# Kernel tuning notes

Hardware: AMD Instinct MI355X
Metric: run time of the kernel (lower is better)

The kernel has to match this reference:

```python
import jax, jax.numpy as jnp
import numpy as np

B, T, N, H, E, K, HOR, OD = 64, 12, 1024, 64, 16, 3, 12, 1
DIN = 1  # input_dim
EPS = 1e-12


def setup_inputs() -> dict:
    key = jax.random.key(0)
    ks = jax.random.split(key, 8)
    s = 0.02
    return {
        "source": jax.random.normal(ks[0], (B, T, N, DIN), jnp.float32),
        "node_emb": jax.random.normal(ks[1], (N, E), jnp.float32),
        "time_emb": jax.random.normal(ks[2], (T, E), jnp.float32),
        "gate_wp": jax.random.normal(ks[3], (E, K, DIN + H, 2 * H), jnp.float32) * s,
        "gate_bp": jax.random.normal(ks[4], (E, 2 * H), jnp.float32) * s,
        "gate_lng": jnp.ones((E,), jnp.float32),
        "gate_lnb": jnp.zeros((E,), jnp.float32),
        "upd_wp": jax.random.normal(ks[5], (E, K, DIN + H, H), jnp.float32) * s,
        "upd_bp": jax.random.normal(ks[6], (E, H), jnp.float32) * s,
        "upd_lng": jnp.ones((E,), jnp.float32),
        "upd_lnb": jnp.zeros((E,), jnp.float32),
        "out_lng": jnp.ones((H,), jnp.float32),
        "out_lnb": jnp.zeros((H,), jnp.float32),
        "conv_w": jax.random.normal(ks[7], (HOR * OD, H), jnp.float32) * s,
        "conv_b": jnp.zeros((HOR * OD,), jnp.float32),
    }


def _ln(x, g, b):
    m = x.mean(-1, keepdims=True)
    v = x.var(-1, keepdims=True)
    return (x - m) / jnp.sqrt(v + EPS) * g + b


def _dagcn(x, node_emb, t_emb, wp, bp, lng, lnb):
    # x: [B, N, C]; node_emb: [N, E]; t_emb: [E] (one timestep)
    e = _ln(node_emb + t_emb[None, :], lng, lnb)          # [N, E] (dropout off in eval)
    sup = jax.nn.softmax(e @ e.T, axis=1)                  # [N, N]
    sl = [jnp.eye(N, dtype=x.dtype), sup]
    for _ in range(2, K):
        sl.append(2.0 * sup @ sl[-1] - sl[-2])             # Chebyshev recursion
    S = jnp.stack(sl, axis=0)                              # [K, N, N]
    w = jnp.einsum('nd,dkio->nkio', e, wp)                 # per-node weights
    bias = e @ bp                                          # [N, O]
    xg = jnp.einsum('knm,bmc->bnkc', S, x)                 # graph conv
    return jnp.einsum('bnki,nkio->bno', xg, w) + bias


def reference(source, node_emb, time_emb, gate_wp, gate_bp, gate_lng, gate_lnb,
              upd_wp, upd_bp, upd_lng, upd_lnb, out_lng, out_lnb, conv_w, conv_b):
    def step(state, xs):
        x_t, te = xs                                        # [B,N,DIN], [E]
        zr = jax.nn.sigmoid(_dagcn(jnp.concatenate([x_t, state], -1),
                                   node_emb, te, gate_wp, gate_bp, gate_lng, gate_lnb))
        z, r = zr[..., :H], zr[..., H:]
        hc = jnp.tanh(_dagcn(jnp.concatenate([x_t, z * state], -1),
                             node_emb, te, upd_wp, upd_bp, upd_lng, upd_lnb))
        h = r * state + (1.0 - r) * hc
        return h, None

    xs = jnp.swapaxes(source, 0, 1)                        # [T,B,N,DIN]
    h0 = jnp.zeros((B, N, H), source.dtype)
    h, _ = jax.lax.scan(step, h0, (xs, time_emb))          # last hidden state [B,N,H]
    y = _ln(h, out_lng, out_lnb)                           # out_dropout off in eval
    out = jnp.einsum('bnh,oh->bon', y, conv_w) + conv_b[None, :, None]  # end_conv
    return out.reshape(B, HOR, OD, N).transpose(0, 1, 3, 2)  # [B,horizon,N,output_dim]
```

## Files before the change

kernel.cpp:

```cpp
#include <hip/hip_runtime.h>
#include <math.h>

namespace {
constexpr int B_ = 64, T_ = 12, N_ = 1024, H_ = 64, E_ = 16;
constexpr int C_  = 65;
constexpr int BC_ = B_ * C_;
constexpr int OG_ = 128;
constexpr int OU_ = 64;
constexpr float EPS_ = 1e-12f;
constexpr int KP_ = 224;
constexpr int COLG_ = OG_ * KP_;
constexpr int COLU_ = OU_ * KP_;
constexpr int NE_ = N_ * E_;
}

typedef unsigned short u16;
typedef unsigned int u32;
using f16x8 = __attribute__((ext_vector_type(8))) _Float16;
using f16x4 = __attribute__((ext_vector_type(4))) _Float16;
using f32x4 = __attribute__((ext_vector_type(4))) float;

__device__ __forceinline__ u32 div65(u32 x) { return (x * 16135u) >> 20; }

__device__ __forceinline__ void gl_lds16(const void* g, void* l, int lane) {
#if __has_builtin(__builtin_amdgcn_global_load_lds)
  __builtin_amdgcn_global_load_lds((const __attribute__((address_space(1))) u32*)g,
                                   (__attribute__((address_space(3))) u32*)l, 16, 0, 0);
#else
  *(uint4*)((char*)l + lane * 16) = *(const uint4*)g;
#endif
}

__device__ __forceinline__ void wprep_body(const float* __restrict__ wp, int NO,
                                           _Float16* __restrict__ wpC, int k, int tid) {
  if (tid >= NO) return;
  f16x8 lo = {}, hi = {};
  if (k < 195) {
    const u32 seg = div65((u32)k);
    const u32 ii = k - seg * 65;
#pragma unroll
    for (int d = 0; d < 8; d++)
      lo[d] = (_Float16)wp[(((size_t)d * 3 + seg) * 65 + ii) * NO + tid];
#pragma unroll
    for (int d = 0; d < 8; d++)
      hi[d] = (_Float16)wp[(((size_t)(d + 8) * 3 + seg) * 65 + ii) * NO + tid];
  }
  _Float16* dst = &wpC[((size_t)tid * KP_ + k) * 16];
  *(f16x8*)dst = lo;
  *(f16x8*)(dst + 8) = hi;
}

__device__ __forceinline__ void sup_body(const float* __restrict__ eT,
                                         _Float16* __restrict__ s16,
                                         int n, int tid, float* red) {
  float en[E_];
#pragma unroll
  for (int d = 0; d < E_; d++) en[d] = eT[d * N_ + n];
  float lg[4];
  float mx = -3.4e38f;
#pragma unroll
  for (int j = 0; j < 4; j++) {
    int m = tid + 256 * j;
    float s = 0.f;
#pragma unroll
    for (int d = 0; d < E_; d++) s = fmaf(en[d], eT[d * N_ + m], s);
    lg[j] = s;
    mx = fmaxf(mx, s);
  }
  red[tid] = mx; __syncthreads();
  for (int off = 128; off > 0; off >>= 1) {
    if (tid < off) red[tid] = fmaxf(red[tid], red[tid + off]);
    __syncthreads();
  }
  mx = red[0]; __syncthreads();
  float sum = 0.f;
#pragma unroll
  for (int j = 0; j < 4; j++) { lg[j] = __expf(lg[j] - mx); sum += lg[j]; }
  red[tid] = sum; __syncthreads();
  for (int off = 128; off > 0; off >>= 1) {
    if (tid < off) red[tid] += red[tid + off];
    __syncthreads();
  }
  float inv = 1.0f / red[0];
#pragma unroll
  for (int j = 0; j < 4; j++)
    s16[(size_t)n * N_ + tid + 256 * j] = (_Float16)(lg[j] * inv);
}

__device__ __forceinline__ void wgen_body(const float* __restrict__ e,
                                          const _Float16* __restrict__ wpC, int COLS,
                                          _Float16* __restrict__ Wt,
                                          int xb, int yb, int tid, float (*es)[16]) {
  const int col0 = xb * 1024 + tid * 4;
  const int n0 = yb * 64;
#pragma unroll
  for (int q = 0; q < 4; q++) {
    int idx = tid + q * 256;
    es[idx >> 4][idx & 15] = e[(size_t)n0 * 16 + idx];
  }
  __syncthreads();
  float wc[4][16];
#pragma unroll
  for (int cc = 0; cc < 4; cc++) {
    f16x8 a = *(const f16x8*)&wpC[(size_t)(col0 + cc) * 16];
    f16x8 b = *(const f16x8*)&wpC[(size_t)(col0 + cc) * 16 + 8];
#pragma unroll
    for (int d = 0; d < 8; d++) { wc[cc][d] = (float)a[d]; wc[cc][8 + d] = (float)b[d]; }
  }
  for (int nn = 0; nn < 64; nn++) {
    float acc[4] = {};
#pragma unroll
    for (int d = 0; d < 16; d++) {
      float ev = es[nn][d];
#pragma unroll
      for (int cc = 0; cc < 4; cc++) acc[cc] = fmaf(ev, wc[cc][d], acc[cc]);
    }
    f16x4 pv;
#pragma unroll
    for (int cc = 0; cc < 4; cc++) pv[cc] = (_Float16)acc[cc];
    *(f16x4*)&Wt[(size_t)(n0 + nn) * COLS + col0] = pv;
  }
}

__device__ __forceinline__ void supT_body(const _Float16* __restrict__ S,
                                          _Float16* __restrict__ ST,
                                          int tile, int tid, _Float16 (*lds)[66]) {
  const int n0 = (tile >> 4) * 64;
  const int m0 = (tile & 15) * 64;
  {
    const int r = tid >> 2, c0 = (tid & 3) * 16;
    const _Float16* sp = &S[(size_t)(n0 + r) * 1024 + m0 + c0];
    f16x8 a = *(const f16x8*)sp;
    f16x8 b = *(const f16x8*)(sp + 8);
#pragma unroll
    for (int i = 0; i < 8; i++) { lds[r][c0 + i] = a[i]; lds[r][c0 + 8 + i] = b[i]; }
  }
  __syncthreads();
  {
    const int c = tid >> 2, r0 = (tid & 3) * 16;
    f16x8 a, b;
#pragma unroll
    for (int i = 0; i < 8; i++) { a[i] = lds[r0 + i][c]; b[i] = lds[r0 + 8 + i][c]; }
    _Float16* dp = &ST[(size_t)(m0 + c) * 1024 + n0 + r0];
    *(f16x8*)dp = a;
    *(f16x8*)(dp + 8) = b;
  }
}

__device__ __forceinline__ void gemm_body(
    const _Float16* __restrict__ A, const _Float16* __restrict__ Bt,
    _Float16* xg, int segoff, int combine, _Float16* __restrict__ rowout,
    int bx, int by, int tid, _Float16* As, _Float16* Bs) {
  const int wave = tid >> 6, lane = tid & 63;
  const int m0 = by * 128, c0 = bx * 64;
  const int lrow = lane >> 3;
  const int lchunk = lane & 7;
  const int fm = lane & 15, fq = lane >> 4;
  f32x4 acc[2][4] = {};
  for (int ks = 0; ks < 16; ks++) {
    const int kp = ks * 64;
#pragma unroll
    for (int q = 0; q < 4; q++) {
      const int seg = wave * 4 + q;
      const int row = seg * 8 + lrow;
      const int sw = lchunk ^ (row & 7);
      gl_lds16(A + (size_t)(m0 + row) * 1024 + kp + sw * 8, &As[seg * 8 * 64], lane);
    }
#pragma unroll
    for (int q = 0; q < 2; q++) {
      const int seg = wave * 2 + q;
      const int row = seg * 8 + lrow;
      const int sw = lchunk ^ (row & 7);
      gl_lds16(Bt + (size_t)(c0 + row) * 1024 + kp + sw * 8, &Bs[seg * 8 * 64], lane);
    }
    __syncthreads();
#pragma unroll
    for (int kk = 0; kk < 2; kk++) {
      f16x8 af[2], bfr[4];
      const int g = kk * 4 + fq;
#pragma unroll
      for (int mt = 0; mt < 2; mt++) {
        const int row = wave * 32 + mt * 16 + fm;
        af[mt] = *(const f16x8*)&As[row * 64 + (g ^ (row & 7)) * 8];
      }
#pragma unroll
      for (int nt = 0; nt < 4; nt++) {
        const int row = nt * 16 + fm;
        bfr[nt] = *(const f16x8*)&Bs[row * 64 + (g ^ (row & 7)) * 8];
      }
#pragma unroll
      for (int mt = 0; mt < 2; mt++)
#pragma unroll
        for (int nt = 0; nt < 4; nt++)
          acc[mt][nt] = __builtin_amdgcn_mfma_f32_16x16x32_f16(af[mt], bfr[nt], acc[mt][nt], 0, 0, 0);
    }
    __syncthreads();
  }
  const int q4 = fq * 4;
#pragma unroll
  for (int nt = 0; nt < 4; nt++) {
    const int col = c0 + nt * 16 + fm;
    if (rowout) {
#pragma unroll
      for (int mt = 0; mt < 2; mt++) {
        const int row = m0 + wave * 32 + mt * 16 + q4;
        const f32x4 v = acc[mt][nt];
#pragma unroll
        for (int j = 0; j < 4; j++)
          rowout[(size_t)(row + j) * 1024 + col] = (_Float16)v[j];
      }
      continue;
    }
    if (col >= BC_) continue;
    const u32 bq = div65((u32)col), cq = (u32)col - bq * 65;
#pragma unroll
    for (int mt = 0; mt < 2; mt++) {
      const int row = m0 + wave * 32 + mt * 16 + q4;
      const f32x4 v = acc[mt][nt];
#pragma unroll
      for (int j = 0; j < 4; j++) {
        size_t base = ((size_t)(row + j) * 64 + bq) * KP_;
        float vv = v[j];
        if (combine) vv = 2.f * vv - (float)xg[base + cq];
        xg[base + segoff + cq] = (_Float16)vv;
      }
    }
  }
}

__global__ __launch_bounds__(256) void k_pre0(
    const float* __restrict__ gate_wp, const float* __restrict__ upd_wp,
    _Float16* __restrict__ wpCg, _Float16* __restrict__ wpCu,
    const float* __restrict__ node_emb, const float* __restrict__ time_emb,
    const float* __restrict__ g_lng, const float* __restrict__ g_lnb,
    const float* __restrict__ u_lng, const float* __restrict__ u_lnb,
    float* __restrict__ eg_all, float* __restrict__ egT_all,
    float* __restrict__ eu_all, float* __restrict__ euT_all) {
  const int bid = blockIdx.x, tid = threadIdx.x;
  if (bid < KP_)     { wprep_body(gate_wp, OG_, wpCg, bid, tid); return; }
  if (bid < 2 * KP_) { wprep_body(upd_wp,  OU_, wpCu, bid - KP_, tid); return; }
  const int idx = bid - 2 * KP_;
  const int t = idx >> 2;
  const int n = (idx & 3) * 256 + tid;
  float v[E_];
  float m = 0.f;
#pragma unroll
  for (int d = 0; d < E_; d++) { v[d] = node_emb[n * E_ + d] + time_emb[t * E_ + d]; m += v[d]; }
  m *= (1.0f / E_);
  float var = 0.f;
#pragma unroll
  for (int d = 0; d < E_; d++) { float x = v[d] - m; var += x * x; }
  var *= (1.0f / E_);
  float rs = rsqrtf(var + EPS_);
#pragma unroll
  for (int d = 0; d < E_; d++) {
    float nv = (v[d] - m) * rs;
    float g = nv * g_lng[d] + g_lnb[d];
    float u = nv * u_lng[d] + u_lnb[d];
    eg_all[(size_t)t * NE_ + n * E_ + d] = g;
    egT_all[(size_t)t * NE_ + d * N_ + n] = g;
    eu_all[(size_t)t * NE_ + n * E_ + d] = u;
    euT_all[(size_t)t * NE_ + d * N_ + n] = u;
  }
}

__global__ __launch_bounds__(256) void k_pro(
    const float* __restrict__ egT0, const float* __restrict__ euT0,
    const float* __restrict__ src,
    _Float16* __restrict__ supG, _Float16* __restrict__ supU0,
    _Float16* __restrict__ Xt, _Float16* __restrict__ xg) {
  __shared__ float red[256];
  const int bid = blockIdx.x, tid = threadIdx.x;
  if (bid < 1024) { sup_body(egT0, supG, bid, tid, red); return; }
  if (bid < 2048) { sup_body(euT0, supU0, bid - 1024, tid, red); return; }
  const int idx = bid - 2048;
  const int b = idx & 63, m0 = (idx >> 6) * 64;
  for (int q = 0; q < 17; q++) {
    int i = tid + q * 256;
    if (i < 64 * 65) {
      int c = i >> 6, m = i & 63;
      float xv = (c == 0) ? src[((size_t)b * T_) * N_ + m0 + m] : 0.f;
      Xt[((size_t)(b * C_ + c)) * 1024 + m0 + m] = (_Float16)xv;
      u32 mm = div65((u32)i), cc = (u32)i - mm * 65;
      float xv2 = (cc == 0) ? src[((size_t)b * T_) * N_ + m0 + mm] : 0.f;
      xg[((size_t)(m0 + mm) * 64 + b) * KP_ + cc] = (_Float16)xv2;
    }
  }
#pragma unroll
  for (int q = 0; q < 8; q++) {
    int i = tid + q * 256;
    int mm = i >> 5, kk = 192 + (i & 31);
    xg[((size_t)(m0 + mm) * 64 + b) * KP_ + kk] = (_Float16)0.f;
  }
}

__global__ __launch_bounds__(256) void k_proT(
    const _Float16* __restrict__ supG0, const _Float16* __restrict__ supU0,
    _Float16* __restrict__ supGT, _Float16* __restrict__ supUT) {
  __shared__ _Float16 lds[64][66];
  const int bid = blockIdx.x;
  if (bid < 256) supT_body(supG0, supGT, bid, threadIdx.x, lds);
  else           supT_body(supU0, supUT, bid - 256, threadIdx.x, lds);
}

__global__ __launch_bounds__(256) void k_pro2(
    const _Float16* __restrict__ supG0, const _Float16* __restrict__ supGT,
    const _Float16* __restrict__ supU0, const _Float16* __restrict__ supUT,
    _Float16* __restrict__ sup2G0, _Float16* __restrict__ sup2U0) {
  __shared__ __align__(16) _Float16 smem[12288];
  const int bid = blockIdx.x, tid = threadIdx.x;
  if (bid < 128)
    gemm_body(supG0, supGT, nullptr, 0, 0, sup2G0, bid % 16, bid / 16, tid, smem, smem + 8192);
  else
    gemm_body(supU0, supUT, nullptr, 0, 0, sup2U0, (bid - 128) % 16, (bid - 128) / 16, tid, smem, smem + 8192);
}

__global__ __launch_bounds__(256) void k_tr(const _Float16* __restrict__ xg,
                                            _Float16* __restrict__ Xt) {
  __shared__ _Float16 tile[64][66];
  const int b = blockIdx.x & 63, m0 = (blockIdx.x >> 6) * 64;
  const int tid = threadIdx.x;
  {
    const int m = tid >> 2, c4 = tid & 3;
    const _Float16* rp = &xg[((size_t)(m0 + m) * 64 + b) * KP_ + c4 * 16];
    f16x8 v0 = *(const f16x8*)rp;
    f16x8 v1 = *(const f16x8*)(rp + 8);
#pragma unroll
    for (int i = 0; i < 8; i++) {
      tile[m][c4 * 16 + i] = v0[i];
      tile[m][c4 * 16 + 8 + i] = v1[i];
    }
    if (c4 == 0) tile[m][64] = rp[64];
  }
  __syncthreads();
  {
    const int m = tid & 63, cg = tid >> 6;
    for (int cc = cg; cc < 65; cc += 4)
      Xt[((size_t)(b * C_ + cc)) * 1024 + m0 + m] = tile[m][cc];
  }
}

__global__ __launch_bounds__(256) void k_ga(
    const _Float16* __restrict__ supG_t, const _Float16* __restrict__ sup2G_t,
    const _Float16* __restrict__ Xt, _Float16* xg,
    const float* __restrict__ eg_t, const _Float16* __restrict__ wpCg,
    _Float16* __restrict__ WtG,
    const float* __restrict__ egT_nx, const float* __restrict__ euT_nx,
    _Float16* __restrict__ supG_nx, _Float16* __restrict__ supU_nx) {
  __shared__ __align__(16) _Float16 smem[12288];
  const int bid = blockIdx.x, tid = threadIdx.x;
  if (bid < 528) {
    gemm_body(supG_t, Xt, xg, 65, 0, nullptr, bid % 66, bid / 66, tid, smem, smem + 8192);
  } else if (bid < 1056) {
    const int w = bid - 528;
    gemm_body(sup2G_t, Xt, xg, 130, 1, nullptr, w % 66, w / 66, tid, smem, smem + 8192);
  } else if (bid < 1504) {
    const int w = bid - 1056;
    wgen_body(eg_t, wpCg, COLG_, WtG, w % 28, w / 28, tid, (float(*)[16])smem);
  } else if (bid < 2528) {
    sup_body(egT_nx, supG_nx, bid - 1504, tid, (float*)smem);
  } else {
    sup_body(euT_nx, supU_nx, bid - 2528, tid, (float*)smem);
  }
}

__global__ __launch_bounds__(256) void k_cgT(
    const float* __restrict__ eg, const _Float16* XG,
    const _Float16* __restrict__ Wt, const float* __restrict__ bp,
    const _Float16* __restrict__ h16, const float* __restrict__ src, int t,
    _Float16* __restrict__ r16, _Float16* xgo,
    const _Float16* __restrict__ supG_nx, const _Float16* __restrict__ supU_nx,
    _Float16* __restrict__ supGT, _Float16* __restrict__ supUT) {
  __shared__ __align__(16) char smraw[19456];
  const int bid = blockIdx.x;
  const int tid = threadIdx.x;
  if (bid >= 1024) {
    _Float16 (*lds)[66] = (_Float16(*)[66])smraw;
    if (bid < 1280) supT_body(supG_nx, supGT, bid - 1024, tid, lds);
    else            supT_body(supU_nx, supUT, bid - 1280, tid, lds);
    return;
  }
  float* es = (float*)smraw;
  float* bias_s = (float*)(smraw + 64);
  _Float16 (*zs)[72] = (_Float16(*)[72])(smraw + 576);
  _Float16 (*rs)[72] = (_Float16(*)[72])(smraw + 9792);
  const int n = bid;
  const int wave = tid >> 6, lane = tid & 63;
  const int fm = lane & 15, fq = lane >> 4;
  const int wm = wave >> 1, wn = wave & 1;
  if (tid < 16) es[tid] = eg[n * 16 + tid];
  __syncthreads();
  if (tid < 128) {
    float bv = 0.f;
#pragma unroll
    for (int d = 0; d < 16; d++) bv = fmaf(es[d], bp[d * OG_ + tid], bv);
    bias_s[tid] = bv;
  }
  const _Float16* Ab = XG + (size_t)n * 64 * KP_;
  const _Float16* Bb = Wt + (size_t)n * OG_ * KP_;
  f16x8 af[2][2], bf[2][4];
#pragma unroll
  for (int mt = 0; mt < 2; mt++)
    af[0][mt] = *(const f16x8*)&Ab[(wm * 32 + mt * 16 + fm) * KP_ + fq * 8];
#pragma unroll
  for (int nt = 0; nt < 4; nt++)
    bf[0][nt] = *(const f16x8*)&Bb[(wn * 64 + nt * 16 + fm) * KP_ + fq * 8];
  f32x4 acc[2][4] = {};
#pragma unroll
  for (int kk = 0; kk < 7; kk++) {
    const int cur = kk & 1;
    if (kk < 6) {
      const int ko = (kk + 1) * 32 + fq * 8;
#pragma unroll
      for (int mt = 0; mt < 2; mt++)
        af[cur ^ 1][mt] = *(const f16x8*)&Ab[(wm * 32 + mt * 16 + fm) * KP_ + ko];
#pragma unroll
      for (int nt = 0; nt < 4; nt++)
        bf[cur ^ 1][nt] = *(const f16x8*)&Bb[(wn * 64 + nt * 16 + fm) * KP_ + ko];
    }
#pragma unroll
    for (int mt = 0; mt < 2; mt++)
#pragma unroll
      for (int nt = 0; nt < 4; nt++)
        acc[mt][nt] = __builtin_amdgcn_mfma_f32_16x16x32_f16(af[cur][mt], bf[cur][nt], acc[mt][nt], 0, 0, 0);
  }
  __syncthreads();
#pragma unroll
  for (int nt = 0; nt < 4; nt++) {
    const int o = wn * 64 + nt * 16 + fm;
    const float bias = bias_s[o];
#pragma unroll
    for (int mt = 0; mt < 2; mt++) {
      const f32x4 v = acc[mt][nt];
#pragma unroll
      for (int j = 0; j < 4; j++) {
        const int b = wm * 32 + mt * 16 + fq * 4 + j;
        float s = 1.0f / (1.0f + __expf(-(v[j] + bias)));
        if (wn == 0) zs[b][o] = (_Float16)s;
        else         rs[b][o - H_] = (_Float16)s;
      }
    }
  }
  __syncthreads();
  {
    const int b = tid >> 2, q = tid & 3;
    const _Float16* hp = &h16[((size_t)b * N_ + n) * H_ + q * 16];
    _Float16* xp = &xgo[((size_t)n * 64 + b) * KP_ + 1 + q * 16];
    _Float16* rp = &r16[((size_t)b * N_ + n) * H_ + q * 16];
    f16x8 r0, r1;
#pragma unroll
    for (int i = 0; i < 8; i++) {
      r0[i] = rs[b][q * 16 + i];
      r1[i] = rs[b][q * 16 + 8 + i];
    }
    *(f16x8*)rp = r0;
    *(f16x8*)(rp + 8) = r1;
    f16x8 h0 = *(const f16x8*)hp;
    f16x8 h1 = *(const f16x8*)(hp + 8);
    f16x8 x0, x1;
#pragma unroll
    for (int i = 0; i < 8; i++) {
      x0[i] = (_Float16)((float)zs[b][q * 16 + i] * (float)h0[i]);
      x1[i] = (_Float16)((float)zs[b][q * 16 + 8 + i] * (float)h1[i]);
    }
    *(f16x8*)xp = x0;
    *(f16x8*)(xp + 8) = x1;
    if (tid < 64) {
      float sv = src[((size_t)tid * T_ + t) * N_ + n];
      xgo[((size_t)n * 64 + tid) * KP_] = (_Float16)sv;
    }
  }
}

__global__ __launch_bounds__(256) void k_gu(
    const _Float16* __restrict__ supU_t, const _Float16* __restrict__ sup2U_t,
    const _Float16* __restrict__ Xt, _Float16* xg,
    const float* __restrict__ eu_t, const _Float16* __restrict__ wpCu,
    _Float16* __restrict__ WtU,
    const _Float16* __restrict__ supG_nx, const _Float16* __restrict__ supGT,
    const _Float16* __restrict__ supU_nx, const _Float16* __restrict__ supUT,
    _Float16* __restrict__ sup2G_nx, _Float16* __restrict__ sup2U_nx) {
  __shared__ __align__(16) _Float16 smem[12288];
  const int bid = blockIdx.x, tid = threadIdx.x;
  if (bid < 528) {
    gemm_body(supU_t, Xt, xg, 65, 0, nullptr, bid % 66, bid / 66, tid, smem, smem + 8192);
  } else if (bid < 1056) {
    const int w = bid - 528;
    gemm_body(sup2U_t, Xt, xg, 130, 1, nullptr, w % 66, w / 66, tid, smem, smem + 8192);
  } else if (bid < 1280) {
    const int w = bid - 1056;
    wgen_body(eu_t, wpCu, COLU_, WtU, w % 14, w / 14, tid, (float(*)[16])smem);
  } else if (bid < 1408) {
    const int w = bid - 1280;
    gemm_body(supG_nx, supGT, nullptr, 0, 0, sup2G_nx, w % 16, w / 16, tid, smem, smem + 8192);
  } else {
    const int w = bid - 1408;
    gemm_body(supU_nx, supUT, nullptr, 0, 0, sup2U_nx, w % 16, w / 16, tid, smem, smem + 8192);
  }
}

__global__ __launch_bounds__(256) void k_cu(
    const float* __restrict__ eu, const _Float16* XG,
    const _Float16* __restrict__ Wt, const float* __restrict__ bp,
    const _Float16* __restrict__ r16, const float* __restrict__ src,
    int t, int donext,
    _Float16* __restrict__ h16, _Float16* xgo) {
  const int n = blockIdx.x;
  const int tid = threadIdx.x;
  const int wave = tid >> 6, lane = tid & 63;
  const int fm = lane & 15, fq = lane >> 4;
  __shared__ float es[16];
  __shared__ float bias_s[64];
  __shared__ _Float16 hs[64][72];
  __shared__ _Float16 rs[64][72];
  if (tid < 16) es[tid] = eu[n * 16 + tid];
  __syncthreads();
  if (tid < 64) {
    float bv = 0.f;
#pragma unroll
    for (int d = 0; d < 16; d++) bv = fmaf(es[d], bp[d * OU_ + tid], bv);
    bias_s[tid] = bv;
  }
  {
    const int b = tid >> 2, q = tid & 3;
    const _Float16* hp = &h16[((size_t)b * N_ + n) * H_ + q * 16];
    const _Float16* rp = &r16[((size_t)b * N_ + n) * H_ + q * 16];
    f16x8 h0 = *(const f16x8*)hp;
    f16x8 h1 = *(const f16x8*)(hp + 8);
    f16x8 r0 = *(const f16x8*)rp;
    f16x8 r1 = *(const f16x8*)(rp + 8);
#pragma unroll
    for (int i = 0; i < 8; i++) {
      hs[b][q * 16 + i] = h0[i];
      hs[b][q * 16 + 8 + i] = h1[i];
      rs[b][q * 16 + i] = r0[i];
      rs[b][q * 16 + 8 + i] = r1[i];
    }
  }
  __syncthreads();
  const _Float16* Ab = XG + (size_t)n * 64 * KP_;
  const _Float16* Bb = Wt + (size_t)n * OU_ * KP_;
  f16x8 af[2], bf[2][4];
  af[0] = *(const f16x8*)&Ab[(wave * 16 + fm) * KP_ + fq * 8];
#pragma unroll
  for (int nt = 0; nt < 4; nt++)
    bf[0][nt] = *(const f16x8*)&Bb[(nt * 16 + fm) * KP_ + fq * 8];
  f32x4 acc[4] = {};
#pragma unroll
  for (int kk = 0; kk < 7; kk++) {
    const int cur = kk & 1;
    if (kk < 6) {
      const int ko = (kk + 1) * 32 + fq * 8;
      af[cur ^ 1] = *(const f16x8*)&Ab[(wave * 16 + fm) * KP_ + ko];
#pragma unroll
      for (int nt = 0; nt < 4; nt++)
        bf[cur ^ 1][nt] = *(const f16x8*)&Bb[(nt * 16 + fm) * KP_ + ko];
    }
#pragma unroll
    for (int nt = 0; nt < 4; nt++)
      acc[nt] = __builtin_amdgcn_mfma_f32_16x16x32_f16(af[cur], bf[cur][nt], acc[nt], 0, 0, 0);
  }
#pragma unroll
  for (int nt = 0; nt < 4; nt++) {
    const int o = nt * 16 + fm;
    const float bias = bias_s[o];
    const f32x4 v = acc[nt];
#pragma unroll
    for (int j = 0; j < 4; j++) {
      const int b = wave * 16 + fq * 4 + j;
      float hc = tanhf(v[j] + bias);
      float rv = (float)rs[b][o];
      float hv = (float)hs[b][o];
      hs[b][o] = (_Float16)(rv * hv + (1.0f - rv) * hc);
    }
  }
  __syncthreads();
  {
    const int b = tid >> 2, q = tid & 3;
    _Float16* hp = &h16[((size_t)b * N_ + n) * H_ + q * 16];
    f16x8 h0, h1;
#pragma unroll
    for (int i = 0; i < 8; i++) {
      h0[i] = hs[b][q * 16 + i];
      h1[i] = hs[b][q * 16 + 8 + i];
    }
    *(f16x8*)hp = h0;
    *(f16x8*)(hp + 8) = h1;
    if (donext) {
      _Float16* xp = &xgo[((size_t)n * 64 + b) * KP_ + 1 + q * 16];
      *(f16x8*)xp = h0;
      *(f16x8*)(xp + 8) = h1;
      if (tid < 64) {
        float sv = src[((size_t)tid * T_ + (t + 1)) * N_ + n];
        xgo[((size_t)n * 64 + tid) * KP_] = (_Float16)sv;
      }
    }
  }
}

__global__ __launch_bounds__(256) void k_final(const _Float16* __restrict__ h16,
                                               const float* __restrict__ out_lng,
                                               const float* __restrict__ out_lnb,
                                               const float* __restrict__ conv_w,
                                               const float* __restrict__ conv_b,
                                               float* __restrict__ out) {
  const int b = blockIdx.x >> 2;
  const int n = (blockIdx.x & 3) * 256 + threadIdx.x;
  __shared__ float cw[12][64];
  __shared__ float cb[12];
  __shared__ float lgs[64], lbs[64];
  for (int idx = threadIdx.x; idx < 12 * 64; idx += 256) cw[idx >> 6][idx & 63] = conv_w[idx];
  if (threadIdx.x < 12) cb[threadIdx.x] = conv_b[threadIdx.x];
  if (threadIdx.x < 64) { lgs[threadIdx.x] = out_lng[threadIdx.x]; lbs[threadIdx.x] = out_lnb[threadIdx.x]; }
  __syncthreads();
  const _Float16* hp = &h16[((size_t)b * N_ + n) * H_];
  float hv[64];
  float mean = 0.f;
#pragma unroll
  for (int i8 = 0; i8 < 8; i8++) {
    f16x8 v = *(const f16x8*)&hp[i8 * 8];
#pragma unroll
    for (int j = 0; j < 8; j++) { hv[i8 * 8 + j] = (float)v[j]; mean += hv[i8 * 8 + j]; }
  }
  mean *= (1.0f / H_);
  float var = 0.f;
#pragma unroll
  for (int i = 0; i < 64; i++) { float d = hv[i] - mean; var += d * d; }
  var *= (1.0f / H_);
  const float rs = rsqrtf(var + EPS_);
  float y[64];
#pragma unroll
  for (int i = 0; i < 64; i++)
    y[i] = (hv[i] - mean) * rs * lgs[i] + lbs[i];
#pragma unroll
  for (int o = 0; o < 12; o++) {
    float acc = cb[o];
#pragma unroll
    for (int i = 0; i < 64; i++) acc = fmaf(y[i], cw[o][i], acc);
    out[((size_t)b * 12 + o) * N_ + n] = acc;
  }
}

extern "C" void kernel_launch(void* const* d_in, const int* in_sizes, int n_in,
                              void* d_out, int out_size, void* d_ws, size_t ws_size,
                              hipStream_t stream) {
  const float* src      = (const float*)d_in[0];
  const float* node_emb = (const float*)d_in[1];
  const float* time_emb = (const float*)d_in[2];
  const float* gate_wp  = (const float*)d_in[3];
  const float* gate_bp  = (const float*)d_in[4];
  const float* gate_lng = (const float*)d_in[5];
  const float* gate_lnb = (const float*)d_in[6];
  const float* upd_wp   = (const float*)d_in[7];
  const float* upd_bp   = (const float*)d_in[8];
  const float* upd_lng  = (const float*)d_in[9];
  const float* upd_lnb  = (const float*)d_in[10];
  const float* out_lng  = (const float*)d_in[11];
  const float* out_lnb  = (const float*)d_in[12];
  const float* conv_w   = (const float*)d_in[13];
  const float* conv_b   = (const float*)d_in[14];
  float* out = (float*)d_out;

  constexpr size_t SZ_H16 = (size_t)B_ * N_ * H_ / 2;
  constexpr size_t SZ_R   = SZ_H16;
  constexpr size_t SZ_T   = (size_t)BC_ * 1024 / 2;
  constexpr size_t SZ_XG  = (size_t)N_ * 64 * KP_ / 2;
  constexpr size_t SZ_WT  = (size_t)N_ * OG_ * KP_ / 2;
  constexpr size_t SZ_WCG = (size_t)COLG_ * 16 / 2;
  constexpr size_t SZ_WCU = (size_t)COLU_ * 16 / 2;
  constexpr size_t SZ_S   = (size_t)N_ * N_ / 2;

  float* ws = (float*)d_ws;
  size_t off = 0;
  float* h16F   = ws + off; off += SZ_H16;
  float* r16F   = ws + off; off += SZ_R;
  float* XtF    = ws + off; off += SZ_T;
  float* xgF    = ws + off; off += SZ_XG;
  float* WtF    = ws + off; off += SZ_WT;
  float* wcgF   = ws + off; off += SZ_WCG;
  float* wcuF   = ws + off; off += SZ_WCU;
  float* supGF  = ws + off; off += 2 * SZ_S;
  float* supUF  = ws + off; off += 2 * SZ_S;
  float* supGTF = ws + off; off += SZ_S;
  float* supUTF = ws + off; off += SZ_S;
  float* s2GF   = ws + off; off += 2 * SZ_S;
  float* s2UF   = ws + off; off += 2 * SZ_S;
  float* eg_all  = ws + off; off += (size_t)T_ * NE_;
  float* egT_all = ws + off; off += (size_t)T_ * NE_;
  float* eu_all  = ws + off; off += (size_t)T_ * NE_;
  float* euT_all = ws + off; off += (size_t)T_ * NE_;
  if (ws_size < off * sizeof(float)) return;

  _Float16* h16   = (_Float16*)h16F;
  _Float16* r16   = (_Float16*)r16F;
  _Float16* Xt    = (_Float16*)XtF;
  _Float16* xg    = (_Float16*)xgF;
  _Float16* WtG   = (_Float16*)WtF;
  _Float16* WtU   = (_Float16*)WtF;
  _Float16* wpCg  = (_Float16*)wcgF;
  _Float16* wpCu  = (_Float16*)wcuF;
  _Float16* supG  = (_Float16*)supGF;
  _Float16* supU  = (_Float16*)supUF;
  _Float16* supGT = (_Float16*)supGTF;
  _Float16* supUT = (_Float16*)supUTF;
  _Float16* s2G   = (_Float16*)s2GF;
  _Float16* s2U   = (_Float16*)s2UF;
  const size_t SB = (size_t)N_ * N_;

  hipMemsetAsync(h16, 0, SZ_H16 * sizeof(float), stream);
  k_pre0<<<2 * KP_ + 48, 256, 0, stream>>>(gate_wp, upd_wp, wpCg, wpCu,
                                           node_emb, time_emb,
                                           gate_lng, gate_lnb, upd_lng, upd_lnb,
                                           eg_all, egT_all, eu_all, euT_all);
  k_pro<<<3072, 256, 0, stream>>>(egT_all, euT_all, src, supG, supU, Xt, xg);
  k_proT<<<512, 256, 0, stream>>>(supG, supU, supGT, supUT);
  k_pro2<<<256, 256, 0, stream>>>(supG, supGT, supU, supUT, s2G, s2U);

  for (int t = 0; t < T_; t++) {
    const int cur = t & 1, nxt = (t + 1) & 1;
    _Float16* supG_t  = supG + (size_t)cur * SB;
    _Float16* supG_nx = supG + (size_t)nxt * SB;
    _Float16* supU_t  = supU + (size_t)cur * SB;
    _Float16* supU_nx = supU + (size_t)nxt * SB;
    _Float16* s2G_t   = s2G + (size_t)cur * SB;
    _Float16* s2G_nx  = s2G + (size_t)nxt * SB;
    _Float16* s2U_t   = s2U + (size_t)cur * SB;
    _Float16* s2U_nx  = s2U + (size_t)nxt * SB;
    const float* eg_t = eg_all + (size_t)t * NE_;
    const float* eu_t = eu_all + (size_t)t * NE_;
    const int more = (t < T_ - 1) ? 1 : 0;
    const int tn = more ? t + 1 : t;

    k_ga<<<more ? 3552 : 1504, 256, 0, stream>>>(
        supG_t, s2G_t, Xt, xg, eg_t, wpCg, WtG,
        egT_all + (size_t)tn * NE_, euT_all + (size_t)tn * NE_, supG_nx, supU_nx);
    k_cgT<<<more ? 1536 : 1024, 256, 0, stream>>>(
        eg_t, xg, WtG, gate_bp, h16, src, t, r16, xg,
        supG_nx, supU_nx, supGT, supUT);
    k_tr<<<1024, 256, 0, stream>>>(xg, Xt);
    k_gu<<<more ? 1536 : 1280, 256, 0, stream>>>(
        supU_t, s2U_t, Xt, xg, eu_t, wpCu, WtU,
        supG_nx, supGT, supU_nx, supUT, s2G_nx, s2U_nx);
    k_cu<<<N_, 256, 0, stream>>>(eu_t, xg, WtU, upd_bp, r16, src, t, more, h16, xg);
    if (more) k_tr<<<1024, 256, 0, stream>>>(xg, Xt);
  }
  k_final<<<B_ * N_ / 256, 256, 0, stream>>>(h16, out_lng, out_lnb, conv_w, conv_b, out);
}
```

Baseline: 1.971 ms.

## Fuse S and S2 graph-conv GEMMs to share the X tile loads

The two separate GEMM block sets (support × X and Chebyshev second-order support × X) become one dual-accumulator GEMM. Each block loads both A matrices and a single shared B (X transposed) tile, then writes both output segments. This halves the global loads and LDS staging of X and removes one set of GEMM blocks from k_ga and k_gu. In exchange it raises LDS use to 40KB and doubles the accumulator registers per thread, which may lower occupancy.

```diff
diff --git a/kernel.cpp b/kernel.cpp
--- a/kernel.cpp
+++ b/kernel.cpp
@@ -149,7 +149,7 @@
 
 __device__ __forceinline__ void gemm_body(
     const _Float16* __restrict__ A, const _Float16* __restrict__ Bt,
-    _Float16* xg, int segoff, int combine, _Float16* __restrict__ rowout,
+    _Float16* __restrict__ rowout,
     int bx, int by, int tid, _Float16* As, _Float16* Bs) {
   const int wave = tid >> 6, lane = tid & 63;
   const int m0 = by * 128, c0 = bx * 64;
@@ -200,29 +200,89 @@
 #pragma unroll
   for (int nt = 0; nt < 4; nt++) {
     const int col = c0 + nt * 16 + fm;
-    if (rowout) {
-#pragma unroll
-      for (int mt = 0; mt < 2; mt++) {
-        const int row = m0 + wave * 32 + mt * 16 + q4;
-        const f32x4 v = acc[mt][nt];
-#pragma unroll
-        for (int j = 0; j < 4; j++)
-          rowout[(size_t)(row + j) * 1024 + col] = (_Float16)v[j];
-      }
-      continue;
-    }
-    if (col >= BC_) continue;
-    const u32 bq = div65((u32)col), cq = (u32)col - bq * 65;
 #pragma unroll
     for (int mt = 0; mt < 2; mt++) {
       const int row = m0 + wave * 32 + mt * 16 + q4;
       const f32x4 v = acc[mt][nt];
 #pragma unroll
+      for (int j = 0; j < 4; j++)
+        rowout[(size_t)(row + j) * 1024 + col] = (_Float16)v[j];
+    }
+  }
+}
+
+__device__ __forceinline__ void gemm2_body(
+    const _Float16* __restrict__ A1, const _Float16* __restrict__ A2,
+    const _Float16* __restrict__ Bt, _Float16* xg,
+    int bx, int by, int tid,
+    _Float16* As1, _Float16* As2, _Float16* Bs) {
+  const int wave = tid >> 6, lane = tid & 63;
+  const int m0 = by * 128, c0 = bx * 64;
+  const int lrow = lane >> 3;
+  const int lchunk = lane & 7;
+  const int fm = lane & 15, fq = lane >> 4;
+  f32x4 acc1[2][4] = {}, acc2[2][4] = {};
+  for (int ks = 0; ks < 16; ks++) {
+    const int kp = ks * 64;
+#pragma unroll
+    for (int q = 0; q < 4; q++) {
+      const int seg = wave * 4 + q;
+      const int row = seg * 8 + lrow;
+      const int sw = lchunk ^ (row & 7);
+      const size_t go = (size_t)(m0 + row) * 1024 + kp + sw * 8;
+      gl_lds16(A1 + go, &As1[seg * 8 * 64], lane);
+      gl_lds16(A2 + go, &As2[seg * 8 * 64], lane);
+    }
+#pragma unroll
+    for (int q = 0; q < 2; q++) {
+      const int seg = wave * 2 + q;
+      const int row = seg * 8 + lrow;
+      const int sw = lchunk ^ (row & 7);
+      gl_lds16(Bt + (size_t)(c0 + row) * 1024 + kp + sw * 8, &Bs[seg * 8 * 64], lane);
+    }
+    __syncthreads();
+#pragma unroll
+    for (int kk = 0; kk < 2; kk++) {
+      f16x8 a1[2], a2[2], bfr[4];
+      const int g = kk * 4 + fq;
+#pragma unroll
+      for (int mt = 0; mt < 2; mt++) {
+        const int row = wave * 32 + mt * 16 + fm;
+        const int o = row * 64 + (g ^ (row & 7)) * 8;
+        a1[mt] = *(const f16x8*)&As1[o];
+        a2[mt] = *(const f16x8*)&As2[o];
+      }
+#pragma unroll
+      for (int nt = 0; nt < 4; nt++) {
+        const int row = nt * 16 + fm;
+        bfr[nt] = *(const f16x8*)&Bs[row * 64 + (g ^ (row & 7)) * 8];
+      }
+#pragma unroll
+      for (int mt = 0; mt < 2; mt++)
+#pragma unroll
+        for (int nt = 0; nt < 4; nt++) {
+          acc1[mt][nt] = __builtin_amdgcn_mfma_f32_16x16x32_f16(a1[mt], bfr[nt], acc1[mt][nt], 0, 0, 0);
+          acc2[mt][nt] = __builtin_amdgcn_mfma_f32_16x16x32_f16(a2[mt], bfr[nt], acc2[mt][nt], 0, 0, 0);
+        }
+    }
+    __syncthreads();
+  }
+  const int q4 = fq * 4;
+#pragma unroll
+  for (int nt = 0; nt < 4; nt++) {
+    const int col = c0 + nt * 16 + fm;
+    if (col >= BC_) continue;
+    const u32 bq = div65((u32)col), cq = (u32)col - bq * 65;
+#pragma unroll
+    for (int mt = 0; mt < 2; mt++) {
+      const int row = m0 + wave * 32 + mt * 16 + q4;
+      const f32x4 v1 = acc1[mt][nt];
+      const f32x4 v2 = acc2[mt][nt];
+#pragma unroll
       for (int j = 0; j < 4; j++) {
         size_t base = ((size_t)(row + j) * 64 + bq) * KP_;
-        float vv = v[j];
-        if (combine) vv = 2.f * vv - (float)xg[base + cq];
-        xg[base + segoff + cq] = (_Float16)vv;
+        xg[base + 65 + cq] = (_Float16)v1[j];
+        xg[base + 130 + cq] = (_Float16)(2.f * v2[j] - (float)xg[base + cq]);
       }
     }
   }
@@ -310,9 +370,9 @@
   __shared__ __align__(16) _Float16 smem[12288];
   const int bid = blockIdx.x, tid = threadIdx.x;
   if (bid < 128)
-    gemm_body(supG0, supGT, nullptr, 0, 0, sup2G0, bid % 16, bid / 16, tid, smem, smem + 8192);
+    gemm_body(supG0, supGT, sup2G0, bid % 16, bid / 16, tid, smem, smem + 8192);
   else
-    gemm_body(supU0, supUT, nullptr, 0, 0, sup2U0, (bid - 128) % 16, (bid - 128) / 16, tid, smem, smem + 8192);
+    gemm_body(supU0, supUT, sup2U0, (bid - 128) % 16, (bid - 128) / 16, tid, smem, smem + 8192);
 }
 
 __global__ __launch_bounds__(256) void k_tr(const _Float16* __restrict__ xg,
@@ -347,20 +407,18 @@
     _Float16* __restrict__ WtG,
     const float* __restrict__ egT_nx, const float* __restrict__ euT_nx,
     _Float16* __restrict__ supG_nx, _Float16* __restrict__ supU_nx) {
-  __shared__ __align__(16) _Float16 smem[12288];
+  __shared__ __align__(16) _Float16 smem[20480];
   const int bid = blockIdx.x, tid = threadIdx.x;
   if (bid < 528) {
-    gemm_body(supG_t, Xt, xg, 65, 0, nullptr, bid % 66, bid / 66, tid, smem, smem + 8192);
-  } else if (bid < 1056) {
+    gemm2_body(supG_t, sup2G_t, Xt, xg, bid % 66, bid / 66, tid,
+               smem, smem + 8192, smem + 16384);
+  } else if (bid < 976) {
     const int w = bid - 528;
-    gemm_body(sup2G_t, Xt, xg, 130, 1, nullptr, w % 66, w / 66, tid, smem, smem + 8192);
-  } else if (bid < 1504) {
-    const int w = bid - 1056;
     wgen_body(eg_t, wpCg, COLG_, WtG, w % 28, w / 28, tid, (float(*)[16])smem);
-  } else if (bid < 2528) {
-    sup_body(egT_nx, supG_nx, bid - 1504, tid, (float*)smem);
+  } else if (bid < 2000) {
+    sup_body(egT_nx, supG_nx, bid - 976, tid, (float*)smem);
   } else {
-    sup_body(euT_nx, supU_nx, bid - 2528, tid, (float*)smem);
+    sup_body(euT_nx, supU_nx, bid - 2000, tid, (float*)smem);
   }
 }
 
@@ -480,22 +538,20 @@
     const _Float16* __restrict__ supG_nx, const _Float16* __restrict__ supGT,
     const _Float16* __restrict__ supU_nx, const _Float16* __restrict__ supUT,
     _Float16* __restrict__ sup2G_nx, _Float16* __restrict__ sup2U_nx) {
-  __shared__ __align__(16) _Float16 smem[12288];
+  __shared__ __align__(16) _Float16 smem[20480];
   const int bid = blockIdx.x, tid = threadIdx.x;
   if (bid < 528) {
-    gemm_body(supU_t, Xt, xg, 65, 0, nullptr, bid % 66, bid / 66, tid, smem, smem + 8192);
-  } else if (bid < 1056) {
+    gemm2_body(supU_t, sup2U_t, Xt, xg, bid % 66, bid / 66, tid,
+               smem, smem + 8192, smem + 16384);
+  } else if (bid < 752) {
     const int w = bid - 528;
-    gemm_body(sup2U_t, Xt, xg, 130, 1, nullptr, w % 66, w / 66, tid, smem, smem + 8192);
-  } else if (bid < 1280) {
-    const int w = bid - 1056;
     wgen_body(eu_t, wpCu, COLU_, WtU, w % 14, w / 14, tid, (float(*)[16])smem);
-  } else if (bid < 1408) {
-    const int w = bid - 1280;
-    gemm_body(supG_nx, supGT, nullptr, 0, 0, sup2G_nx, w % 16, w / 16, tid, smem, smem + 8192);
+  } else if (bid < 880) {
+    const int w = bid - 752;
+    gemm_body(supG_nx, supGT, sup2G_nx, w % 16, w / 16, tid, smem, smem + 8192);
   } else {
-    const int w = bid - 1408;
-    gemm_body(supU_nx, supUT, nullptr, 0, 0, sup2U_nx, w % 16, w / 16, tid, smem, smem + 8192);
+    const int w = bid - 880;
+    gemm_body(supU_nx, supUT, sup2U_nx, w % 16, w / 16, tid, smem, smem + 8192);
   }
 }
 
@@ -731,14 +787,14 @@
     const int more = (t < T_ - 1) ? 1 : 0;
     const int tn = more ? t + 1 : t;
 
-    k_ga<<<more ? 3552 : 1504, 256, 0, stream>>>(
+    k_ga<<<more ? 3024 : 976, 256, 0, stream>>>(
         supG_t, s2G_t, Xt, xg, eg_t, wpCg, WtG,
         egT_all + (size_t)tn * NE_, euT_all + (size_t)tn * NE_, supG_nx, supU_nx);
     k_cgT<<<more ? 1536 : 1024, 256, 0, stream>>>(
         eg_t, xg, WtG, gate_bp, h16, src, t, r16, xg,
         supG_nx, supU_nx, supGT, supUT);
     k_tr<<<1024, 256, 0, stream>>>(xg, Xt);
-    k_gu<<<more ? 1536 : 1280, 256, 0, stream>>>(
+    k_gu<<<more ? 1008 : 752, 256, 0, stream>>>(
         supU_t, s2U_t, Xt, xg, eu_t, wpCu, WtU,
         supG_nx, supGT, supU_nx, supUT, s2G_nx, s2U_nx);
     k_cu<<<N_, 256, 0, stream>>>(eu_t, xg, WtU, upd_bp, r16, src, t, more, h16, xg);
```

Measured after the change: 2.098 ms. +6.4%, slower.
